# Kernel optimization log

Hardware: AMD Instinct MI355X
Metric: run time of the kernel (lower is better)

Reference implementation:

```python
import jax, jax.numpy as jnp
import numpy as np

B, S, D, H = 2, 2048, 1024, 16
HD = D // H

def setup_inputs() -> dict:
    key = jax.random.key(0)
    ks = jax.random.split(key, 5)
    s = 1.0 / np.sqrt(D)
    return {
        "x": jax.random.normal(ks[0], (B, S, D), dtype=jnp.float32),
        "Wq": jax.random.normal(ks[1], (D, D), dtype=jnp.float32) * s,
        "Wk": jax.random.normal(ks[2], (D, D), dtype=jnp.float32) * s,
        "Wv": jax.random.normal(ks[3], (D, D), dtype=jnp.float32) * s,
        "Wo": jax.random.normal(ks[4], (D, D), dtype=jnp.float32) * s,
        "bo": jnp.zeros((D,), dtype=jnp.float32),
    }

def reference(x, Wq, Wk, Wv, Wo, bo):
    b, n, _ = x.shape
    # QKV projections (no bias), reshape to [B, H, S, HD]
    def proj(W):
        return (x @ W.T).reshape(b, n, H, HD).transpose(0, 2, 1, 3)
    q, k, v = proj(Wq), proj(Wk), proj(Wv)
    scores = jnp.einsum("bhqd,bhkd->bhqk", q, k)
    causal = jnp.triu(jnp.ones((n, n), dtype=bool), k=1)
    scores = jnp.where(causal, -jnp.inf, scores)
    attn = jax.nn.softmax(scores / np.sqrt(HD), axis=-1)  # dropout p=0.0 (eval)
    ctx = jnp.einsum("bhqk,bhkd->bhqd", attn, v)
    ctx = ctx.transpose(0, 2, 1, 3).reshape(b, n, D)
    return ctx @ Wo.T + bo
```

## Files before the change

### kernel.cpp

```cpp
#include <hip/hip_runtime.h>
#include <stdint.h>


typedef __bf16 bf16_t;
typedef __bf16 bf16x8 __attribute__((ext_vector_type(8)));
typedef float  f32x4  __attribute__((ext_vector_type(4)));
typedef uint32_t u32x4 __attribute__((ext_vector_type(4)));

#define MFMA16(A, B, C) __builtin_amdgcn_mfma_f32_16x16x32_bf16(A, B, C, 0, 0, 0)

__device__ __forceinline__ void async_ld16(const bf16_t* g, bf16_t* l) {
  __builtin_amdgcn_global_load_lds(
      (const __attribute__((address_space(1))) void*)g,
      (__attribute__((address_space(3))) void*)l, 16, 0, 0);
}

__device__ __forceinline__ u32x4 ld8(const float* p) {
  const float4 a = *(const float4*)p;
  const float4 b = *(const float4*)(p + 4);
  union { u32x4 v; bf16_t h[8]; } r;
  r.h[0] = (bf16_t)a.x; r.h[1] = (bf16_t)a.y;
  r.h[2] = (bf16_t)a.z; r.h[3] = (bf16_t)a.w;
  r.h[4] = (bf16_t)b.x; r.h[5] = (bf16_t)b.y;
  r.h[6] = (bf16_t)b.z; r.h[7] = (bf16_t)b.w;
  return r.v;
}

__global__ __launch_bounds__(256) void cvt_all(
    const float* __restrict__ sx, const float* __restrict__ s1,
    const float* __restrict__ s2, const float* __restrict__ s3,
    bf16_t* __restrict__ dx, bf16_t* __restrict__ d1,
    bf16_t* __restrict__ d2, bf16_t* __restrict__ d3) {
  const int y = blockIdx.y;
  if (y != 0 && blockIdx.x >= 1024) return;
  const int i4 = (blockIdx.x * 256 + threadIdx.x) * 4;
  const float* s = (y == 0) ? sx : (y == 1) ? s1 : (y == 2) ? s2 : s3;
  bf16_t*      d = (y == 0) ? dx : (y == 1) ? d1 : (y == 2) ? d2 : d3;
  const float4 v = *(const float4*)(s + i4);
  union { uint64_t u; bf16_t h[4]; } pk;
  pk.h[0] = (bf16_t)v.x; pk.h[1] = (bf16_t)v.y;
  pk.h[2] = (bf16_t)v.z; pk.h[3] = (bf16_t)v.w;
  *(uint64_t*)(d + i4) = pk.u;
}

__global__ __launch_bounds__(256, 2) void gemm_qkv_a(
    const bf16_t* __restrict__ X,  const bf16_t* __restrict__ Wq,
    const bf16_t* __restrict__ Wk, const bf16_t* __restrict__ Wv,
    bf16_t* __restrict__ Q, bf16_t* __restrict__ K, bf16_t* __restrict__ V) {
  const int z = blockIdx.z;
  const bf16_t* W = (z == 0) ? Wq : (z == 1) ? Wk : Wv;
  bf16_t*       D = (z == 0) ? Q  : (z == 1) ? K  : V;
  const int mode = (z == 2) ? 1 : 0;

  __shared__ __align__(16) bf16_t As[128 * 64];
  __shared__ __align__(16) bf16_t Bs[128 * 64];

  const int tid  = threadIdx.x;
  const int lane = tid & 63;
  const int w    = tid >> 6;
  const int quad = lane >> 4;
  const int l15  = lane & 15;
  const int bm   = blockIdx.y * 128;
  const int bn   = blockIdx.x * 128;
  const int wm   = (w >> 1) * 64;
  const int wn   = (w & 1) * 64;
  const int sr   = lane >> 3;
  const int sc   = lane & 7;

  f32x4 acc[4][4] = {};

  for (int k0 = 0; k0 < 1024; k0 += 64) {
#pragma unroll
    for (int j = 0; j < 4; ++j) {
      const int r0 = w * 32 + j * 8;
      const int r  = r0 + sr;
      const int c  = sc ^ (r & 7);
      async_ld16(X + (size_t)(bm + r) * 1024 + k0 + c * 8, &As[r0 * 64]);
      async_ld16(W + (size_t)(bn + r) * 1024 + k0 + c * 8, &Bs[r0 * 64]);
    }
    __syncthreads();
#pragma unroll
    for (int kk = 0; kk < 64; kk += 32) {
      const int ck = (kk >> 3) + quad;
      bf16x8 aF[4], bF[4];
#pragma unroll
      for (int mt = 0; mt < 4; ++mt) {
        const int r = wm + mt * 16 + l15;
        aF[mt] = *(const bf16x8*)&As[r * 64 + (ck ^ (r & 7)) * 8];
      }
#pragma unroll
      for (int nt = 0; nt < 4; ++nt) {
        const int r = wn + nt * 16 + l15;
        bF[nt] = *(const bf16x8*)&Bs[r * 64 + (ck ^ (r & 7)) * 8];
      }
#pragma unroll
      for (int mt = 0; mt < 4; ++mt)
#pragma unroll
        for (int nt = 0; nt < 4; ++nt)
          acc[mt][nt] = MFMA16(aF[mt], bF[nt], acc[mt][nt]);
    }
    __syncthreads();
  }

#pragma unroll
  for (int mt = 0; mt < 4; ++mt) {
#pragma unroll
    for (int nt = 0; nt < 4; ++nt) {
      const int n  = bn + wn + nt * 16 + l15;
      const int mb = bm + wm + mt * 16 + quad * 4;
      const int h = n >> 6, hd = n & 63;
      if (mode == 0) {
#pragma unroll
        for (int r = 0; r < 4; ++r) {
          const int m = mb + r;
          const int b = m >> 11, s = m & 2047;
          D[(size_t)b * 2097152 + (size_t)h * 131072 + (size_t)s * 64 + hd] =
              (bf16_t)acc[mt][nt][r];
        }
      } else {
        const int b = mb >> 11, s0 = mb & 2047;
        union { uint64_t u; bf16_t h4[4]; } pk;
#pragma unroll
        for (int r = 0; r < 4; ++r) pk.h4[r] = (bf16_t)acc[mt][nt][r];
        *(uint64_t*)(D + (size_t)b * 2097152 + (size_t)h * 131072 +
                     (size_t)hd * 2048 + s0) = pk.u;
      }
    }
  }
}

__global__ __launch_bounds__(256, 2) void gemm_out_m(
    const bf16_t* __restrict__ ctx, const float* __restrict__ Wo,
    float* __restrict__ out, const float* __restrict__ bo) {
  __shared__ __align__(16) bf16_t As[64 * 64];
  __shared__ __align__(16) bf16_t Bs[128 * 64];

  const int tid  = threadIdx.x;
  const int lane = tid & 63;
  const int w    = tid >> 6;
  const int quad = lane >> 4;
  const int l15  = lane & 15;
  const int bm   = blockIdx.y * 64;
  const int bn   = blockIdx.x * 128;
  const int wm   = (w >> 1) * 32;
  const int wn   = (w & 1) * 64;
  const int sr   = lane >> 3;
  const int sc   = lane & 7;
  const int srow = tid >> 3;
  const int schk = tid & 7;

  f32x4 acc[2][4] = {};

  for (int k0 = 0; k0 < 1024; k0 += 64) {
#pragma unroll
    for (int j = 0; j < 2; ++j) {
      const int r0 = w * 16 + j * 8;
      const int r  = r0 + sr;
      const int c  = sc ^ (r & 7);
      async_ld16(ctx + (size_t)(bm + r) * 1024 + k0 + c * 8, &As[r0 * 64]);
    }
    u32x4 rb[4];
#pragma unroll
    for (int s2 = 0; s2 < 4; ++s2) {
      const int r = srow + s2 * 32;
      rb[s2] = ld8(Wo + (size_t)(bn + r) * 1024 + k0 + schk * 8);
    }
#pragma unroll
    for (int s2 = 0; s2 < 4; ++s2) {
      const int r = srow + s2 * 32;
      *(u32x4*)&Bs[r * 64 + ((schk ^ (r & 7)) * 8)] = rb[s2];
    }
    __syncthreads();
#pragma unroll
    for (int kk = 0; kk < 64; kk += 32) {
      const int ck = (kk >> 3) + quad;
      bf16x8 aF[2], bF[4];
#pragma unroll
      for (int mt = 0; mt < 2; ++mt) {
        const int r = wm + mt * 16 + l15;
        aF[mt] = *(const bf16x8*)&As[r * 64 + (ck ^ (r & 7)) * 8];
      }
#pragma unroll
      for (int nt = 0; nt < 4; ++nt) {
        const int r = wn + nt * 16 + l15;
        bF[nt] = *(const bf16x8*)&Bs[r * 64 + (ck ^ (r & 7)) * 8];
      }
#pragma unroll
      for (int mt = 0; mt < 2; ++mt)
#pragma unroll
        for (int nt = 0; nt < 4; ++nt)
          acc[mt][nt] = MFMA16(aF[mt], bF[nt], acc[mt][nt]);
    }
    __syncthreads();
  }

#pragma unroll
  for (int mt = 0; mt < 2; ++mt) {
#pragma unroll
    for (int nt = 0; nt < 4; ++nt) {
      const int n  = bn + wn + nt * 16 + l15;
      const int mb = bm + wm + mt * 16 + quad * 4;
      const float bv = bo[n];
#pragma unroll
      for (int r = 0; r < 4; ++r)
        out[(size_t)(mb + r) * 1024 + n] = acc[mt][nt][r] + bv;
    }
  }
}

__global__ __launch_bounds__(256, 2) void attn(
    const bf16_t* __restrict__ Qw, const bf16_t* __restrict__ Kw,
    const bf16_t* __restrict__ Vw, bf16_t* __restrict__ ctx) {
  constexpr int LDK = 72, LDV = 136, LDP = 136;
  __shared__ __align__(16) bf16_t Ks[128 * LDK];
  __shared__ __align__(16) bf16_t Vts[64 * LDV];
  __shared__ __align__(16) bf16_t Ps[128 * LDP];

  const int tid  = threadIdx.x;
  const int lane = tid & 63;
  const int w    = tid >> 6;
  const int quad = lane >> 4;
  const int l15  = lane & 15;
  const int b    = blockIdx.z;
  const int qt   = (b == 0) ? blockIdx.x : 15 - blockIdx.x;
  const int h    = blockIdx.y;
  const size_t bh = (size_t)(b * 16 + h) * (size_t)(2048 * 64);
  const bf16_t* Qh = Qw + bh;
  const bf16_t* Kh = Kw + bh;
  const bf16_t* Vh = Vw + bh;

  const int srow = tid >> 3, schk = tid & 7;
  const int vrow = tid >> 4, vchk = tid & 15;

  bf16_t* Qs = Ps;
  {
    u32x4 rq[4];
#pragma unroll
    for (int s2 = 0; s2 < 4; ++s2)
      rq[s2] = *(const u32x4*)(Qh + (size_t)(qt * 128 + srow + s2 * 32) * 64 + schk * 8);
#pragma unroll
    for (int s2 = 0; s2 < 4; ++s2)
      *(u32x4*)&Qs[(srow + s2 * 32) * LDK + schk * 8] = rq[s2];
  }
  __syncthreads();
  bf16x8 qF[2][2];
#pragma unroll
  for (int kq = 0; kq < 2; ++kq)
#pragma unroll
    for (int k2 = 0; k2 < 2; ++k2)
      qF[kq][k2] = *(const bf16x8*)
          &Qs[(w * 32 + kq * 16 + l15) * LDK + k2 * 32 + quad * 8];

  f32x4 O[2][4] = {};
  float mrow[2] = {-1e30f, -1e30f};
  float lrow[2] = {0.f, 0.f};

  const float sc_log2 = 0.125f * 1.44269504088896340736f;

  u32x4 rk[4], rv[4];
#pragma unroll
  for (int s2 = 0; s2 < 4; ++s2)
    rk[s2] = *(const u32x4*)(Kh + (size_t)(srow + s2 * 32) * 64 + schk * 8);
#pragma unroll
  for (int s2 = 0; s2 < 4; ++s2)
    rv[s2] = *(const u32x4*)(Vh + (size_t)(vrow + s2 * 16) * 2048 + vchk * 8);

  for (int kt = 0; kt <= qt; ++kt) {
    __syncthreads();
#pragma unroll
    for (int s2 = 0; s2 < 4; ++s2)
      *(u32x4*)&Ks[(srow + s2 * 32) * LDK + schk * 8] = rk[s2];
#pragma unroll
    for (int s2 = 0; s2 < 4; ++s2)
      *(u32x4*)&Vts[(vrow + s2 * 16) * LDV + vchk * 8] = rv[s2];
    __syncthreads();

    if (kt < qt) {
      const int kn = kt + 1;
#pragma unroll
      for (int s2 = 0; s2 < 4; ++s2)
        rk[s2] = *(const u32x4*)(Kh + (size_t)(kn * 128 + srow + s2 * 32) * 64 + schk * 8);
#pragma unroll
      for (int s2 = 0; s2 < 4; ++s2)
        rv[s2] = *(const u32x4*)(Vh + (size_t)(vrow + s2 * 16) * 2048 + kn * 128 + vchk * 8);
    }

    f32x4 St[2][8] = {};
#pragma unroll
    for (int ntk = 0; ntk < 8; ++ntk) {
      const int kr = ntk * 16 + l15;
#pragma unroll
      for (int k2 = 0; k2 < 2; ++k2) {
        const bf16x8 kF = *(const bf16x8*)&Ks[kr * LDK + k2 * 32 + quad * 8];
#pragma unroll
        for (int kq = 0; kq < 2; ++kq)
          St[kq][ntk] = MFMA16(kF, qF[kq][k2], St[kq][ntk]);
      }
    }

    if (kt == qt) {
#pragma unroll
      for (int kq = 0; kq < 2; ++kq) {
        const int ql = w * 32 + kq * 16 + l15;
#pragma unroll
        for (int ntk = 0; ntk < 8; ++ntk)
#pragma unroll
          for (int r = 0; r < 4; ++r)
            if (ntk * 16 + quad * 4 + r > ql) St[kq][ntk][r] = -1e30f;
      }
    }

    float aq[2];
#pragma unroll
    for (int kq = 0; kq < 2; ++kq) {
      float mx = -1e30f;
#pragma unroll
      for (int ntk = 0; ntk < 8; ++ntk)
#pragma unroll
        for (int r = 0; r < 4; ++r) mx = fmaxf(mx, St[kq][ntk][r]);
      mx = fmaxf(mx, __shfl_xor(mx, 16));
      mx = fmaxf(mx, __shfl_xor(mx, 32));
      const float mnew  = fmaxf(mrow[kq], mx);
      const float alpha = exp2f((mrow[kq] - mnew) * sc_log2);
      mrow[kq] = mnew;
      float rs = 0.f;
#pragma unroll
      for (int ntk = 0; ntk < 8; ++ntk) {
        union { uint64_t u; bf16_t h4[4]; } pk;
#pragma unroll
        for (int r = 0; r < 4; ++r) {
          const float p = exp2f((St[kq][ntk][r] - mnew) * sc_log2);
          rs += p;
          pk.h4[r] = (bf16_t)p;
        }
        *(uint64_t*)&Ps[(w * 32 + kq * 16 + l15) * LDP + ntk * 16 + quad * 4] = pk.u;
      }
      rs += __shfl_xor(rs, 16);
      rs += __shfl_xor(rs, 32);
      lrow[kq] = lrow[kq] * alpha + rs;
      aq[kq] = alpha;
    }

#pragma unroll
    for (int mt = 0; mt < 2; ++mt) {
#pragma unroll
      for (int r = 0; r < 4; ++r) {
        const float a = __shfl(aq[mt], quad * 4 + r);
#pragma unroll
        for (int nt = 0; nt < 4; ++nt) O[mt][nt][r] *= a;
      }
    }

#pragma unroll
    for (int kk = 0; kk < 128; kk += 32) {
      const int co = kk + quad * 8;
      bf16x8 pF[2], vF[4];
#pragma unroll
      for (int mt = 0; mt < 2; ++mt)
        pF[mt] = *(const bf16x8*)&Ps[(w * 32 + mt * 16 + l15) * LDP + co];
#pragma unroll
      for (int nt = 0; nt < 4; ++nt)
        vF[nt] = *(const bf16x8*)&Vts[(nt * 16 + l15) * LDV + co];
#pragma unroll
      for (int mt = 0; mt < 2; ++mt)
#pragma unroll
        for (int nt = 0; nt < 4; ++nt)
          O[mt][nt] = MFMA16(pF[mt], vF[nt], O[mt][nt]);
    }
  }

#pragma unroll
  for (int mt = 0; mt < 2; ++mt) {
#pragma unroll
    for (int r = 0; r < 4; ++r) {
      const float lr = __shfl(lrow[mt], quad * 4 + r);
      const float iv = 1.f / lr;
      const int s = qt * 128 + w * 32 + mt * 16 + quad * 4 + r;
#pragma unroll
      for (int nt = 0; nt < 4; ++nt) {
        const int hd = nt * 16 + l15;
        ctx[(size_t)(b * 2048 + s) * 1024 + h * 64 + hd] =
            (bf16_t)(O[mt][nt][r] * iv);
      }
    }
  }
}

extern "C" void kernel_launch(void* const* d_in, const int* in_sizes, int n_in,
                              void* d_out, int out_size, void* d_ws, size_t ws_size,
                              hipStream_t stream) {
  const float* x  = (const float*)d_in[0];
  const float* Wq = (const float*)d_in[1];
  const float* Wk = (const float*)d_in[2];
  const float* Wv = (const float*)d_in[3];
  const float* Wo = (const float*)d_in[4];
  const float* bo = (const float*)d_in[5];

  bf16_t* ws   = (bf16_t*)d_ws;
  bf16_t* Qw   = ws;
  bf16_t* Kw   = ws + 4194304;
  bf16_t* Vw   = ws + 8388608;
  bf16_t* ctxw = ws + 12582912;

  bf16_t* dscr = (bf16_t*)d_out;
  bf16_t* xb   = dscr;
  bf16_t* Wqb  = dscr + 4194304;
  bf16_t* Wkb  = dscr + 5242880;
  bf16_t* Wvb  = dscr + 6291456;
  float*  out  = (float*)d_out;

  dim3 blk(256);
  cvt_all<<<dim3(4096, 4), blk, 0, stream>>>(x, Wq, Wk, Wv, xb, Wqb, Wkb, Wvb);
  gemm_qkv_a<<<dim3(8, 32, 3), blk, 0, stream>>>(xb, Wqb, Wkb, Wvb, Qw, Kw, Vw);
  attn<<<dim3(16, 16, 2), blk, 0, stream>>>(Qw, Kw, Vw, ctxw);
  gemm_out_m<<<dim3(8, 64), blk, 0, stream>>>(ctxw, Wo, out, bo);
}
```

Baseline: 187.1 us.

## Rewrite attention with 32x32 MFMA, async double-buffered K/V, register-resident P

Restructures the flash-attention kernel to use 32x32x16 bf16 MFMAs. K/V tiles are loaded with global_load_lds into double-buffered, XOR-swizzled LDS, so the next tile streams in while the current one is computed. The P matrix stays in registers and is reshuffled with permlane32_swap instead of round-tripping through LDS. It also adds a lazy rescale that skips the O rescale when the running max grows by no more than a threshold. This removes the LDS stores of P and K/V and some barriers, at the cost of more register pressure and relying on vmcnt counting being correct.

```diff
diff --git a/kernel.cpp b/kernel.cpp
--- a/kernel.cpp
+++ b/kernel.cpp
@@ -5,14 +5,21 @@
 typedef __bf16 bf16_t;
 typedef __bf16 bf16x8 __attribute__((ext_vector_type(8)));
 typedef float  f32x4  __attribute__((ext_vector_type(4)));
+typedef float  f32x16 __attribute__((ext_vector_type(16)));
 typedef uint32_t u32x4 __attribute__((ext_vector_type(4)));
+typedef uint32_t u32x2 __attribute__((ext_vector_type(2)));
 
 #define MFMA16(A, B, C) __builtin_amdgcn_mfma_f32_16x16x32_bf16(A, B, C, 0, 0, 0)
+#define MFMA32(A, B, C) __builtin_amdgcn_mfma_f32_32x32x16_bf16(A, B, C, 0, 0, 0)
 
 __device__ __forceinline__ void async_ld16(const bf16_t* g, bf16_t* l) {
   __builtin_amdgcn_global_load_lds(
       (const __attribute__((address_space(1))) void*)g,
       (__attribute__((address_space(3))) void*)l, 16, 0, 0);
+}
+
+__device__ __forceinline__ u32x2 pl32swap(uint32_t x, uint32_t y) {
+  return __builtin_amdgcn_permlane32_swap(x, y, false, false);
 }
 
 __device__ __forceinline__ u32x4 ld8(const float* p) {
@@ -211,16 +218,14 @@
 __global__ __launch_bounds__(256, 2) void attn(
     const bf16_t* __restrict__ Qw, const bf16_t* __restrict__ Kw,
     const bf16_t* __restrict__ Vw, bf16_t* __restrict__ ctx) {
-  constexpr int LDK = 72, LDV = 136, LDP = 136;
-  __shared__ __align__(16) bf16_t Ks[128 * LDK];
-  __shared__ __align__(16) bf16_t Vts[64 * LDV];
-  __shared__ __align__(16) bf16_t Ps[128 * LDP];
+  __shared__ __align__(16) bf16_t Kb[2][128 * 64];
+  __shared__ __align__(16) bf16_t Vb[2][64 * 128];
 
   const int tid  = threadIdx.x;
   const int lane = tid & 63;
   const int w    = tid >> 6;
-  const int quad = lane >> 4;
-  const int l15  = lane & 15;
+  const int l31  = lane & 31;
+  const int hi   = lane >> 5;
   const int b    = blockIdx.z;
   const int qt   = (b == 0) ? blockIdx.x : 15 - blockIdx.x;
   const int h    = blockIdx.y;
@@ -229,159 +234,158 @@
   const bf16_t* Kh = Kw + bh;
   const bf16_t* Vh = Vw + bh;
 
-  const int srow = tid >> 3, schk = tid & 7;
-  const int vrow = tid >> 4, vchk = tid & 15;
-
-  bf16_t* Qs = Ps;
+  bf16x8 qF[4];
   {
-    u32x4 rq[4];
-#pragma unroll
-    for (int s2 = 0; s2 < 4; ++s2)
-      rq[s2] = *(const u32x4*)(Qh + (size_t)(qt * 128 + srow + s2 * 32) * 64 + schk * 8);
-#pragma unroll
-    for (int s2 = 0; s2 < 4; ++s2)
-      *(u32x4*)&Qs[(srow + s2 * 32) * LDK + schk * 8] = rq[s2];
-  }
-  __syncthreads();
-  bf16x8 qF[2][2];
-#pragma unroll
-  for (int kq = 0; kq < 2; ++kq)
-#pragma unroll
-    for (int k2 = 0; k2 < 2; ++k2)
-      qF[kq][k2] = *(const bf16x8*)
-          &Qs[(w * 32 + kq * 16 + l15) * LDK + k2 * 32 + quad * 8];
-
-  f32x4 O[2][4] = {};
-  float mrow[2] = {-1e30f, -1e30f};
-  float lrow[2] = {0.f, 0.f};
-
+    const bf16_t* qrow = Qh + (size_t)(qt * 128 + w * 32 + l31) * 64 + hi * 8;
+#pragma unroll
+    for (int t2 = 0; t2 < 4; ++t2) qF[t2] = *(const bf16x8*)(qrow + t2 * 16);
+  }
+
+  const int krl = lane >> 3, kcl = lane & 7;
+  const int vrl = lane >> 4, vcl = lane & 15;
+
+  {
+#pragma unroll
+    for (int j = 0; j < 4; ++j) {
+      const int r0 = w * 32 + j * 8;
+      const int r  = r0 + krl;
+      async_ld16(Kh + (size_t)r * 64 + (kcl ^ (r & 7)) * 8, &Kb[0][r0 * 64]);
+    }
+#pragma unroll
+    for (int j = 0; j < 4; ++j) {
+      const int r0 = w * 16 + j * 4;
+      const int r  = r0 + vrl;
+      async_ld16(Vh + (size_t)r * 2048 + (vcl ^ (r & 7)) * 8, &Vb[0][r0 * 128]);
+    }
+  }
+
+  f32x16 O[2] = {};
+  float mrow = -1e30f, lrow = 0.f;
   const float sc_log2 = 0.125f * 1.44269504088896340736f;
-
-  u32x4 rk[4], rv[4];
-#pragma unroll
-  for (int s2 = 0; s2 < 4; ++s2)
-    rk[s2] = *(const u32x4*)(Kh + (size_t)(srow + s2 * 32) * 64 + schk * 8);
-#pragma unroll
-  for (int s2 = 0; s2 < 4; ++s2)
-    rv[s2] = *(const u32x4*)(Vh + (size_t)(vrow + s2 * 16) * 2048 + vchk * 8);
+  const float DTHR = 44.0f;
 
   for (int kt = 0; kt <= qt; ++kt) {
-    __syncthreads();
-#pragma unroll
-    for (int s2 = 0; s2 < 4; ++s2)
-      *(u32x4*)&Ks[(srow + s2 * 32) * LDK + schk * 8] = rk[s2];
-#pragma unroll
-    for (int s2 = 0; s2 < 4; ++s2)
-      *(u32x4*)&Vts[(vrow + s2 * 16) * LDV + vchk * 8] = rv[s2];
-    __syncthreads();
-
+    const int cur = kt & 1;
+    asm volatile("" ::: "memory");
+    __builtin_amdgcn_s_barrier();
+    asm volatile("" ::: "memory");
     if (kt < qt) {
       const int kn = kt + 1;
 #pragma unroll
-      for (int s2 = 0; s2 < 4; ++s2)
-        rk[s2] = *(const u32x4*)(Kh + (size_t)(kn * 128 + srow + s2 * 32) * 64 + schk * 8);
-#pragma unroll
-      for (int s2 = 0; s2 < 4; ++s2)
-        rv[s2] = *(const u32x4*)(Vh + (size_t)(vrow + s2 * 16) * 2048 + kn * 128 + vchk * 8);
-    }
-
-    f32x4 St[2][8] = {};
-#pragma unroll
-    for (int ntk = 0; ntk < 8; ++ntk) {
-      const int kr = ntk * 16 + l15;
-#pragma unroll
-      for (int k2 = 0; k2 < 2; ++k2) {
-        const bf16x8 kF = *(const bf16x8*)&Ks[kr * LDK + k2 * 32 + quad * 8];
-#pragma unroll
-        for (int kq = 0; kq < 2; ++kq)
-          St[kq][ntk] = MFMA16(kF, qF[kq][k2], St[kq][ntk]);
+      for (int j = 0; j < 4; ++j) {
+        const int r0 = w * 32 + j * 8;
+        const int r  = r0 + krl;
+        async_ld16(Kh + (size_t)(kn * 128 + r) * 64 + (kcl ^ (r & 7)) * 8,
+                   &Kb[cur ^ 1][r0 * 64]);
+      }
+#pragma unroll
+      for (int j = 0; j < 4; ++j) {
+        const int r0 = w * 16 + j * 4;
+        const int r  = r0 + vrl;
+        async_ld16(Vh + (size_t)r * 2048 + kn * 128 + (vcl ^ (r & 7)) * 8,
+                   &Vb[cur ^ 1][r0 * 128]);
+      }
+      asm volatile("s_waitcnt vmcnt(8)" ::: "memory");
+    } else {
+      asm volatile("s_waitcnt vmcnt(0)" ::: "memory");
+    }
+    __builtin_amdgcn_s_barrier();
+    asm volatile("" ::: "memory");
+
+    f32x16 St[4] = {};
+#pragma unroll
+    for (int c = 0; c < 4; ++c) {
+      const int kr = c * 32 + l31;
+      const bf16_t* kbase = &Kb[cur][kr * 64];
+      const int sw = kr & 7;
+#pragma unroll
+      for (int t2 = 0; t2 < 4; ++t2) {
+        const bf16x8 kF = *(const bf16x8*)(kbase + (((t2 << 1) | hi) ^ sw) * 8);
+        St[c] = MFMA32(kF, qF[t2], St[c]);
       }
     }
 
     if (kt == qt) {
 #pragma unroll
-      for (int kq = 0; kq < 2; ++kq) {
-        const int ql = w * 32 + kq * 16 + l15;
-#pragma unroll
-        for (int ntk = 0; ntk < 8; ++ntk)
-#pragma unroll
-          for (int r = 0; r < 4; ++r)
-            if (ntk * 16 + quad * 4 + r > ql) St[kq][ntk][r] = -1e30f;
-      }
-    }
-
-    float aq[2];
-#pragma unroll
-    for (int kq = 0; kq < 2; ++kq) {
-      float mx = -1e30f;
-#pragma unroll
-      for (int ntk = 0; ntk < 8; ++ntk)
-#pragma unroll
-        for (int r = 0; r < 4; ++r) mx = fmaxf(mx, St[kq][ntk][r]);
-      mx = fmaxf(mx, __shfl_xor(mx, 16));
-      mx = fmaxf(mx, __shfl_xor(mx, 32));
-      const float mnew  = fmaxf(mrow[kq], mx);
-      const float alpha = exp2f((mrow[kq] - mnew) * sc_log2);
-      mrow[kq] = mnew;
-      float rs = 0.f;
-#pragma unroll
-      for (int ntk = 0; ntk < 8; ++ntk) {
-        union { uint64_t u; bf16_t h4[4]; } pk;
-#pragma unroll
-        for (int r = 0; r < 4; ++r) {
-          const float p = exp2f((St[kq][ntk][r] - mnew) * sc_log2);
-          rs += p;
-          pk.h4[r] = (bf16_t)p;
+      for (int c = 0; c < 4; ++c)
+#pragma unroll
+        for (int g = 0; g < 4; ++g)
+#pragma unroll
+          for (int r2 = 0; r2 < 4; ++r2)
+            if (c * 32 + g * 8 + hi * 4 + r2 > w * 32 + l31)
+              St[c][g * 4 + r2] = -1e30f;
+    }
+
+    float mx = -1e30f;
+#pragma unroll
+    for (int c = 0; c < 4; ++c)
+#pragma unroll
+      for (int rg = 0; rg < 16; ++rg) mx = fmaxf(mx, St[c][rg]);
+    mx = fmaxf(mx, __shfl_xor(mx, 32));
+
+    float alpha = 1.f;
+    if (!__all(mx - mrow <= DTHR)) {
+      const float mnew = fmaxf(mrow, mx);
+      alpha = exp2f((mrow - mnew) * sc_log2);
+      mrow = mnew;
+#pragma unroll
+      for (int g = 0; g < 4; ++g)
+#pragma unroll
+        for (int r2 = 0; r2 < 4; ++r2) {
+          const float a = __shfl(alpha, g * 8 + hi * 4 + r2);
+          O[0][g * 4 + r2] *= a;
+          O[1][g * 4 + r2] *= a;
         }
-        *(uint64_t*)&Ps[(w * 32 + kq * 16 + l15) * LDP + ntk * 16 + quad * 4] = pk.u;
-      }
-      rs += __shfl_xor(rs, 16);
-      rs += __shfl_xor(rs, 32);
-      lrow[kq] = lrow[kq] * alpha + rs;
-      aq[kq] = alpha;
-    }
-
-#pragma unroll
-    for (int mt = 0; mt < 2; ++mt) {
-#pragma unroll
-      for (int r = 0; r < 4; ++r) {
-        const float a = __shfl(aq[mt], quad * 4 + r);
-#pragma unroll
-        for (int nt = 0; nt < 4; ++nt) O[mt][nt][r] *= a;
-      }
-    }
-
-#pragma unroll
-    for (int kk = 0; kk < 128; kk += 32) {
-      const int co = kk + quad * 8;
-      bf16x8 pF[2], vF[4];
-#pragma unroll
-      for (int mt = 0; mt < 2; ++mt)
-        pF[mt] = *(const bf16x8*)&Ps[(w * 32 + mt * 16 + l15) * LDP + co];
-#pragma unroll
-      for (int nt = 0; nt < 4; ++nt)
-        vF[nt] = *(const bf16x8*)&Vts[(nt * 16 + l15) * LDV + co];
-#pragma unroll
-      for (int mt = 0; mt < 2; ++mt)
-#pragma unroll
-        for (int nt = 0; nt < 4; ++nt)
-          O[mt][nt] = MFMA16(pF[mt], vF[nt], O[mt][nt]);
-    }
-  }
-
-#pragma unroll
-  for (int mt = 0; mt < 2; ++mt) {
-#pragma unroll
-    for (int r = 0; r < 4; ++r) {
-      const float lr = __shfl(lrow[mt], quad * 4 + r);
+    }
+
+    const float mb = mrow * sc_log2;
+    float rs = 0.f;
+#pragma unroll
+    for (int c = 0; c < 4; ++c) {
+      uint32_t pk0[4], pk1[4];
+#pragma unroll
+      for (int g = 0; g < 4; ++g) {
+        const float p0 = exp2f(St[c][g * 4 + 0] * sc_log2 - mb);
+        const float p1 = exp2f(St[c][g * 4 + 1] * sc_log2 - mb);
+        const float p2 = exp2f(St[c][g * 4 + 2] * sc_log2 - mb);
+        const float p3 = exp2f(St[c][g * 4 + 3] * sc_log2 - mb);
+        rs += (p0 + p1) + (p2 + p3);
+        union { uint32_t u; bf16_t h2[2]; } a0, a1;
+        a0.h2[0] = (bf16_t)p0; a0.h2[1] = (bf16_t)p1;
+        a1.h2[0] = (bf16_t)p2; a1.h2[1] = (bf16_t)p3;
+        pk0[g] = a0.u; pk1[g] = a1.u;
+      }
+#pragma unroll
+      for (int tl = 0; tl < 2; ++tl) {
+        const u32x2 s0 = pl32swap(pk0[2 * tl], pk0[2 * tl + 1]);
+        const u32x2 s1 = pl32swap(pk1[2 * tl], pk1[2 * tl + 1]);
+        union { u32x4 u4; bf16x8 h8; } fr;
+        fr.u4 = u32x4{s0[0], s1[0], s0[1], s1[1]};
+        const int t = c * 2 + tl;
+#pragma unroll
+        for (int nb = 0; nb < 2; ++nb) {
+          const int vr = nb * 32 + l31;
+          const bf16x8 vF = *(const bf16x8*)
+              &Vb[cur][vr * 128 + ((((t << 1) | hi) ^ (vr & 7)) * 8)];
+          O[nb] = MFMA32(fr.h8, vF, O[nb]);
+        }
+      }
+    }
+    rs += __shfl_xor(rs, 32);
+    lrow = lrow * alpha + rs;
+  }
+
+#pragma unroll
+  for (int g = 0; g < 4; ++g) {
+#pragma unroll
+    for (int r2 = 0; r2 < 4; ++r2) {
+      const int qrow = g * 8 + hi * 4 + r2;
+      const float lr = __shfl(lrow, qrow);
       const float iv = 1.f / lr;
-      const int s = qt * 128 + w * 32 + mt * 16 + quad * 4 + r;
-#pragma unroll
-      for (int nt = 0; nt < 4; ++nt) {
-        const int hd = nt * 16 + l15;
-        ctx[(size_t)(b * 2048 + s) * 1024 + h * 64 + hd] =
-            (bf16_t)(O[mt][nt][r] * iv);
-      }
+      const int s = qt * 128 + w * 32 + qrow;
+      bf16_t* crow = ctx + (size_t)(b * 2048 + s) * 1024 + h * 64 + l31;
+      crow[0]  = (bf16_t)(O[0][g * 4 + r2] * iv);
+      crow[32] = (bf16_t)(O[1][g * 4 + r2] * iv);
     }
   }
 }
```

New measurement: 190.5 us. About the same (+1.8%).

## Shrink attention tiles to 64x64, add lazy rescaling and MFMA priority

Applied to the files above, without the earlier changes.

The attention kernel now processes 64-query by 64-key tiles instead of 128x128. That doubles the grid, cuts LDS use, and raises the occupancy target to 4 blocks per CU. Tile order is permuted across batch and head halves to balance the causal workload. Online-softmax rescaling of the output accumulators is skipped unless the running max grows past a threshold, and s_setprio is raised around the MFMA loops. Smaller tiles mean more K/V reloads per query and more barriers per unit of work.

```diff
diff --git a/kernel.cpp b/kernel.cpp
--- a/kernel.cpp
+++ b/kernel.cpp
@@ -208,180 +208,168 @@
   }
 }
 
-__global__ __launch_bounds__(256, 2) void attn(
+__global__ __launch_bounds__(256, 4) void attn(
     const bf16_t* __restrict__ Qw, const bf16_t* __restrict__ Kw,
     const bf16_t* __restrict__ Vw, bf16_t* __restrict__ ctx) {
-  constexpr int LDK = 72, LDV = 136, LDP = 136;
-  __shared__ __align__(16) bf16_t Ks[128 * LDK];
+  constexpr int LDK = 72, LDV = 72, LDP = 72;
+  __shared__ __align__(16) bf16_t Ks[64 * LDK];
   __shared__ __align__(16) bf16_t Vts[64 * LDV];
-  __shared__ __align__(16) bf16_t Ps[128 * LDP];
+  __shared__ __align__(16) bf16_t Ps[64 * LDP];
 
   const int tid  = threadIdx.x;
   const int lane = tid & 63;
   const int w    = tid >> 6;
   const int quad = lane >> 4;
   const int l15  = lane & 15;
+  const int h    = blockIdx.y;
   const int b    = blockIdx.z;
-  const int qt   = (b == 0) ? blockIdx.x : 15 - blockIdx.x;
-  const int h    = blockIdx.y;
+  const int x    = blockIdx.x;
+  const int u    = (b << 1) | ((h >> 3) & 1);
+  const int r64  = (u == 0) ? x
+                 : (u == 1) ? (31 - x)
+                 : (u == 2) ? ((x + 16) & 31)
+                            : ((15 - x) & 31);
   const size_t bh = (size_t)(b * 16 + h) * (size_t)(2048 * 64);
   const bf16_t* Qh = Qw + bh;
   const bf16_t* Kh = Kw + bh;
   const bf16_t* Vh = Vw + bh;
 
-  const int srow = tid >> 3, schk = tid & 7;
-  const int vrow = tid >> 4, vchk = tid & 15;
-
-  bf16_t* Qs = Ps;
+  const int srl = lane >> 3, scl = lane & 7;
+
   {
-    u32x4 rq[4];
-#pragma unroll
-    for (int s2 = 0; s2 < 4; ++s2)
-      rq[s2] = *(const u32x4*)(Qh + (size_t)(qt * 128 + srow + s2 * 32) * 64 + schk * 8);
-#pragma unroll
-    for (int s2 = 0; s2 < 4; ++s2)
-      *(u32x4*)&Qs[(srow + s2 * 32) * LDK + schk * 8] = rq[s2];
+    const int srow = tid >> 3, sch = tid & 7;
+    u32x4 rq[2];
+#pragma unroll
+    for (int s2 = 0; s2 < 2; ++s2)
+      rq[s2] = *(const u32x4*)(Qh + (size_t)(r64 * 64 + srow + s2 * 32) * 64 + sch * 8);
+#pragma unroll
+    for (int s2 = 0; s2 < 2; ++s2)
+      *(u32x4*)&Ps[(srow + s2 * 32) * LDP + sch * 8] = rq[s2];
   }
   __syncthreads();
-  bf16x8 qF[2][2];
-#pragma unroll
-  for (int kq = 0; kq < 2; ++kq)
-#pragma unroll
-    for (int k2 = 0; k2 < 2; ++k2)
-      qF[kq][k2] = *(const bf16x8*)
-          &Qs[(w * 32 + kq * 16 + l15) * LDK + k2 * 32 + quad * 8];
-
-  f32x4 O[2][4] = {};
-  float mrow[2] = {-1e30f, -1e30f};
-  float lrow[2] = {0.f, 0.f};
-
+  bf16x8 qF[2];
+#pragma unroll
+  for (int k2 = 0; k2 < 2; ++k2)
+    qF[k2] = *(const bf16x8*)&Ps[(w * 16 + l15) * LDP + k2 * 32 + quad * 8];
+
+  f32x4 O[4] = {};
+  float mrow = -1e30f, lrow = 0.f;
   const float sc_log2 = 0.125f * 1.44269504088896340736f;
-
-  u32x4 rk[4], rv[4];
-#pragma unroll
-  for (int s2 = 0; s2 < 4; ++s2)
-    rk[s2] = *(const u32x4*)(Kh + (size_t)(srow + s2 * 32) * 64 + schk * 8);
-#pragma unroll
-  for (int s2 = 0; s2 < 4; ++s2)
-    rv[s2] = *(const u32x4*)(Vh + (size_t)(vrow + s2 * 16) * 2048 + vchk * 8);
-
-  for (int kt = 0; kt <= qt; ++kt) {
-    __syncthreads();
-#pragma unroll
-    for (int s2 = 0; s2 < 4; ++s2)
-      *(u32x4*)&Ks[(srow + s2 * 32) * LDK + schk * 8] = rk[s2];
-#pragma unroll
-    for (int s2 = 0; s2 < 4; ++s2)
-      *(u32x4*)&Vts[(vrow + s2 * 16) * LDV + vchk * 8] = rv[s2];
-    __syncthreads();
-
-    if (kt < qt) {
+  const float DTHR = 44.0f;
+
+  u32x4 rk[2], rv[2];
+#pragma unroll
+  for (int j = 0; j < 2; ++j)
+    rk[j] = *(const u32x4*)(Kh + (size_t)(w * 16 + j * 8 + srl) * 64 + scl * 8);
+#pragma unroll
+  for (int j = 0; j < 2; ++j)
+    rv[j] = *(const u32x4*)(Vh + (size_t)(w * 16 + j * 8 + srl) * 2048 + scl * 8);
+
+  for (int kt = 0; kt <= r64; ++kt) {
+    __syncthreads();
+#pragma unroll
+    for (int j = 0; j < 2; ++j)
+      *(u32x4*)&Ks[(w * 16 + j * 8 + srl) * LDK + scl * 8] = rk[j];
+#pragma unroll
+    for (int j = 0; j < 2; ++j)
+      *(u32x4*)&Vts[(w * 16 + j * 8 + srl) * LDV + scl * 8] = rv[j];
+    __syncthreads();
+
+    if (kt < r64) {
       const int kn = kt + 1;
 #pragma unroll
-      for (int s2 = 0; s2 < 4; ++s2)
-        rk[s2] = *(const u32x4*)(Kh + (size_t)(kn * 128 + srow + s2 * 32) * 64 + schk * 8);
-#pragma unroll
-      for (int s2 = 0; s2 < 4; ++s2)
-        rv[s2] = *(const u32x4*)(Vh + (size_t)(vrow + s2 * 16) * 2048 + kn * 128 + vchk * 8);
-    }
-
-    f32x4 St[2][8] = {};
-#pragma unroll
-    for (int ntk = 0; ntk < 8; ++ntk) {
+      for (int j = 0; j < 2; ++j)
+        rk[j] = *(const u32x4*)(Kh + (size_t)(kn * 64 + w * 16 + j * 8 + srl) * 64 + scl * 8);
+#pragma unroll
+      for (int j = 0; j < 2; ++j)
+        rv[j] = *(const u32x4*)(Vh + (size_t)(w * 16 + j * 8 + srl) * 2048 + kn * 64 + scl * 8);
+    }
+
+    f32x4 St[4] = {};
+    __builtin_amdgcn_s_setprio(1);
+#pragma unroll
+    for (int ntk = 0; ntk < 4; ++ntk) {
       const int kr = ntk * 16 + l15;
 #pragma unroll
       for (int k2 = 0; k2 < 2; ++k2) {
         const bf16x8 kF = *(const bf16x8*)&Ks[kr * LDK + k2 * 32 + quad * 8];
-#pragma unroll
-        for (int kq = 0; kq < 2; ++kq)
-          St[kq][ntk] = MFMA16(kF, qF[kq][k2], St[kq][ntk]);
-      }
-    }
-
-    if (kt == qt) {
-#pragma unroll
-      for (int kq = 0; kq < 2; ++kq) {
-        const int ql = w * 32 + kq * 16 + l15;
-#pragma unroll
-        for (int ntk = 0; ntk < 8; ++ntk)
-#pragma unroll
-          for (int r = 0; r < 4; ++r)
-            if (ntk * 16 + quad * 4 + r > ql) St[kq][ntk][r] = -1e30f;
-      }
-    }
-
-    float aq[2];
-#pragma unroll
-    for (int kq = 0; kq < 2; ++kq) {
-      float mx = -1e30f;
-#pragma unroll
-      for (int ntk = 0; ntk < 8; ++ntk)
-#pragma unroll
-        for (int r = 0; r < 4; ++r) mx = fmaxf(mx, St[kq][ntk][r]);
-      mx = fmaxf(mx, __shfl_xor(mx, 16));
-      mx = fmaxf(mx, __shfl_xor(mx, 32));
-      const float mnew  = fmaxf(mrow[kq], mx);
-      const float alpha = exp2f((mrow[kq] - mnew) * sc_log2);
-      mrow[kq] = mnew;
-      float rs = 0.f;
-#pragma unroll
-      for (int ntk = 0; ntk < 8; ++ntk) {
-        union { uint64_t u; bf16_t h4[4]; } pk;
-#pragma unroll
-        for (int r = 0; r < 4; ++r) {
-          const float p = exp2f((St[kq][ntk][r] - mnew) * sc_log2);
-          rs += p;
-          pk.h4[r] = (bf16_t)p;
-        }
-        *(uint64_t*)&Ps[(w * 32 + kq * 16 + l15) * LDP + ntk * 16 + quad * 4] = pk.u;
-      }
-      rs += __shfl_xor(rs, 16);
-      rs += __shfl_xor(rs, 32);
-      lrow[kq] = lrow[kq] * alpha + rs;
-      aq[kq] = alpha;
-    }
-
-#pragma unroll
-    for (int mt = 0; mt < 2; ++mt) {
+        St[ntk] = MFMA16(kF, qF[k2], St[ntk]);
+      }
+    }
+    __builtin_amdgcn_s_setprio(0);
+
+    if (kt == r64) {
+      const int ql = w * 16 + l15;
+#pragma unroll
+      for (int ntk = 0; ntk < 4; ++ntk)
+#pragma unroll
+        for (int r = 0; r < 4; ++r)
+          if (ntk * 16 + quad * 4 + r > ql) St[ntk][r] = -1e30f;
+    }
+
+    float mx = -1e30f;
+#pragma unroll
+    for (int ntk = 0; ntk < 4; ++ntk)
+#pragma unroll
+      for (int r = 0; r < 4; ++r) mx = fmaxf(mx, St[ntk][r]);
+    mx = fmaxf(mx, __shfl_xor(mx, 16));
+    mx = fmaxf(mx, __shfl_xor(mx, 32));
+
+    float alpha = 1.f;
+    if (!__all(mx - mrow <= DTHR)) {
+      const float mnew = fmaxf(mrow, mx);
+      alpha = exp2f((mrow - mnew) * sc_log2);
+      mrow = mnew;
 #pragma unroll
       for (int r = 0; r < 4; ++r) {
-        const float a = __shfl(aq[mt], quad * 4 + r);
-#pragma unroll
-        for (int nt = 0; nt < 4; ++nt) O[mt][nt][r] *= a;
-      }
-    }
-
-#pragma unroll
-    for (int kk = 0; kk < 128; kk += 32) {
+        const float a = __shfl(alpha, quad * 4 + r);
+#pragma unroll
+        for (int nt = 0; nt < 4; ++nt) O[nt][r] *= a;
+      }
+    }
+
+    float rs = 0.f;
+#pragma unroll
+    for (int ntk = 0; ntk < 4; ++ntk) {
+      union { uint64_t u64; bf16_t h4[4]; } pk;
+#pragma unroll
+      for (int r = 0; r < 4; ++r) {
+        const float p = exp2f((St[ntk][r] - mrow) * sc_log2);
+        rs += p;
+        pk.h4[r] = (bf16_t)p;
+      }
+      *(uint64_t*)&Ps[(w * 16 + l15) * LDP + ntk * 16 + quad * 4] = pk.u64;
+    }
+    rs += __shfl_xor(rs, 16);
+    rs += __shfl_xor(rs, 32);
+    lrow = lrow * alpha + rs;
+
+    __builtin_amdgcn_s_setprio(1);
+#pragma unroll
+    for (int kk = 0; kk < 64; kk += 32) {
       const int co = kk + quad * 8;
-      bf16x8 pF[2], vF[4];
-#pragma unroll
-      for (int mt = 0; mt < 2; ++mt)
-        pF[mt] = *(const bf16x8*)&Ps[(w * 32 + mt * 16 + l15) * LDP + co];
+      const bf16x8 pF = *(const bf16x8*)&Ps[(w * 16 + l15) * LDP + co];
+      bf16x8 vF[4];
 #pragma unroll
       for (int nt = 0; nt < 4; ++nt)
         vF[nt] = *(const bf16x8*)&Vts[(nt * 16 + l15) * LDV + co];
 #pragma unroll
-      for (int mt = 0; mt < 2; ++mt)
-#pragma unroll
-        for (int nt = 0; nt < 4; ++nt)
-          O[mt][nt] = MFMA16(pF[mt], vF[nt], O[mt][nt]);
-    }
-  }
-
-#pragma unroll
-  for (int mt = 0; mt < 2; ++mt) {
-#pragma unroll
-    for (int r = 0; r < 4; ++r) {
-      const float lr = __shfl(lrow[mt], quad * 4 + r);
-      const float iv = 1.f / lr;
-      const int s = qt * 128 + w * 32 + mt * 16 + quad * 4 + r;
-#pragma unroll
-      for (int nt = 0; nt < 4; ++nt) {
-        const int hd = nt * 16 + l15;
-        ctx[(size_t)(b * 2048 + s) * 1024 + h * 64 + hd] =
-            (bf16_t)(O[mt][nt][r] * iv);
-      }
+      for (int nt = 0; nt < 4; ++nt)
+        O[nt] = MFMA16(pF, vF[nt], O[nt]);
+    }
+    __builtin_amdgcn_s_setprio(0);
+  }
+
+#pragma unroll
+  for (int r = 0; r < 4; ++r) {
+    const float lr = __shfl(lrow, quad * 4 + r);
+    const float iv = 1.f / lr;
+    const int s = r64 * 64 + w * 16 + quad * 4 + r;
+#pragma unroll
+    for (int nt = 0; nt < 4; ++nt) {
+      const int hd = nt * 16 + l15;
+      ctx[(size_t)(b * 2048 + s) * 1024 + h * 64 + hd] =
+          (bf16_t)(O[nt][r] * iv);
     }
   }
 }
@@ -412,6 +400,6 @@
   dim3 blk(256);
   cvt_all<<<dim3(4096, 4), blk, 0, stream>>>(x, Wq, Wk, Wv, xb, Wqb, Wkb, Wvb);
   gemm_qkv_a<<<dim3(8, 32, 3), blk, 0, stream>>>(xb, Wqb, Wkb, Wvb, Qw, Kw, Vw);
-  attn<<<dim3(16, 16, 2), blk, 0, stream>>>(Qw, Kw, Vw, ctxw);
+  attn<<<dim3(32, 16, 2), blk, 0, stream>>>(Qw, Kw, Vw, ctxw);
   gemm_out_m<<<dim3(8, 64), blk, 0, stream>>>(ctxw, Wo, out, bo);
 }
```

Measured after the change: 187.3 us. About the same (+0.1%).
